# Kernel tuning notes

Hardware: AMD Instinct MI355X
Metric: run time of the kernel (lower is better)

The kernel has to match this reference:

```python
import jax, jax.numpy as jnp
import numpy as np

D = 48; N_IN = 8192; K = 24; RADIUS = 0.033
C_HID = 86; C_IN = 5; EMB = 16; MODES = 6; PAD = 6; N_LAYERS = 4
EPS = 1e-5


def _pos_embed(x):
    # neuraloperator PositionalEmbedding: scalar -> EMB channels (cos || sin)
    half = EMB // 2
    freqs = (1.0 / 10000.0) ** (jnp.arange(half, dtype=x.dtype) / half)
    ang = x[:, None] * freqs[None, :]
    return jnp.concatenate([jnp.cos(ang), jnp.sin(ang)], axis=-1)


def _gelu(x):
    return jax.nn.gelu(x, approximate=False)


def _conv1x1(h, w, b):
    return jnp.einsum('oi,ixyz->oxyz', w, h) + b[:, None, None, None]


def _group_norm(h, w, b):
    # GroupNorm(num_groups=1) on a batch-1 [C,X,Y,Z] tensor
    mu = jnp.mean(h)
    var = jnp.var(h)
    hn = (h - mu) * jax.lax.rsqrt(var + EPS)
    return hn * w[:, None, None, None] + b[:, None, None, None]


def _spectral_conv(h, wr, wi):
    S = h.shape[1]
    Xf = jnp.fft.rfftn(h, axes=(1, 2, 3))  # [C,S,S,S//2+1] complex64
    W = wr + 1j * wi                        # [4,C,C,m,m,m]
    out = jnp.zeros_like(Xf)
    m = MODES
    sls = (slice(0, m), slice(-m, None))
    c = 0
    for a in range(2):
        for b in range(2):
            blk = Xf[:, sls[a], sls[b], :m]
            res = jnp.einsum('ixyz,ioxyz->oxyz', blk, W[c])
            out = out.at[:, sls[a], sls[b], :m].set(res)
            c += 1
    return jnp.fft.irfftn(out, s=(S, S, S), axes=(1, 2, 3))


def _forward(x_in, x_out, df, w_lift, b_lift, spec_wr, spec_wi,
             w_skip, b_skip, mlp1_w, mlp1_b, mlp2_w, mlp2_b, wms, bms,
             g1_w, g1_b, g2_w, g2_b, k1_w, k1_b, k2_w, k2_b, k3_w, k3_b,
             p1_w, p1_b, p2_w, p2_b, nb_idx, nb_mask):
    n_out = D ** 3
    x_out_embed = _pos_embed(x_out.reshape(-1)).reshape(n_out, 3 * EMB)
    feat = jnp.concatenate([df, jnp.transpose(x_out, (3, 0, 1, 2))], axis=0)  # [5,D,D,D]
    h = _conv1x1(feat, w_lift, b_lift)
    h = jnp.pad(h, ((0, 0), (0, PAD), (0, PAD), (0, PAD)))  # one-sided domain padding
    for l in range(N_LAYERS):
        skip = _conv1x1(h, w_skip[l], b_skip[l])
        hf = _group_norm(_spectral_conv(h, spec_wr[l], spec_wi[l]), g1_w[l], g1_b[l])
        h = hf + skip
        if l < N_LAYERS - 1:
            h = _gelu(h)
        mskip = _conv1x1(h, wms[l], bms[l])
        hm = _conv1x1(_gelu(_conv1x1(h, mlp1_w[l], mlp1_b[l])), mlp2_w[l], mlp2_b[l])
        hm = _group_norm(hm, g2_w[l], g2_b[l])
        h = hm + mskip
        if l < N_LAYERS - 1:
            h = _gelu(h)
    h = h[:, :D, :D, :D]
    f_y = h.reshape(C_HID, n_out).T  # [n_out, C_HID]
    x_in_embed = _pos_embed(x_in.reshape(-1)).reshape(N_IN, 3 * EMB)
    # GNO: gather -> kernel MLP -> elementwise (linear kernel) -> mean scatter-reduce
    y_g = x_out_embed[nb_idx]                                        # [N,K,48]
    q_g = jnp.broadcast_to(x_in_embed[:, None, :], (N_IN, K, 3 * EMB))
    kin = jnp.concatenate([y_g, q_g], axis=-1)                       # [N,K,96]
    k = _gelu(kin @ k1_w.T + k1_b)
    k = _gelu(k @ k2_w.T + k2_b)
    k = k @ k3_w.T + k3_b                                            # [N,K,C_HID]
    f_g = f_y[nb_idx]                                                # [N,K,C_HID]
    mask = nb_mask[..., None].astype(k.dtype)
    num = jnp.sum(k * f_g * mask, axis=1)
    den = jnp.maximum(jnp.sum(nb_mask, axis=1), 1).astype(k.dtype)[:, None]
    out = num / den
    out = _gelu(out @ p1_w.T + p1_b)
    return out @ p2_w.T + p2_b                                       # [N,1]


def setup_inputs():
    rng = np.random.default_rng(0)
    lin = np.linspace(0.0, 1.0, D, dtype=np.float32)
    gx, gy, gz = np.meshgrid(lin, lin, lin, indexing='ij')
    x_out = np.stack([gx, gy, gz], axis=-1)                          # [D,D,D,3]
    x_in = rng.random((N_IN, 3)).astype(np.float32)
    # --- host-side ball-query neighbor search (regular grid, radius=RADIUS) ---
    spacing = 1.0 / (D - 1)
    rc = int(np.ceil(RADIUS / spacing))
    offs = np.arange(-rc, rc + 1)
    oi, oj, ok = np.meshgrid(offs, offs, offs, indexing='ij')
    offsets = np.stack([oi.ravel(), oj.ravel(), ok.ravel()], axis=-1)
    base = np.floor(x_in / spacing + 0.5).astype(np.int64)
    cand = base[:, None, :] + offsets[None, :, :]
    ok_v = np.all((cand >= 0) & (cand < D), axis=-1)
    cand = np.clip(cand, 0, D - 1)
    d2 = np.sum((cand.astype(np.float32) * spacing - x_in[:, None, :]) ** 2, axis=-1)
    inball = ok_v & (d2 <= RADIUS ** 2)
    order = np.argsort(~inball, axis=1, kind='stable')[:, :K]
    flat = (cand[..., 0] * D + cand[..., 1]) * D + cand[..., 2]
    nb_idx = np.take_along_axis(flat, order, axis=1).astype(np.int32)
    nb_mask = np.take_along_axis(inball, order, axis=1)

    def lw(o, i):
        return jnp.asarray((rng.standard_normal((o, i)) / np.sqrt(i)).astype(np.float32))

    def slw(n, o, i):
        return jnp.asarray((rng.standard_normal((n, o, i)) / np.sqrt(i)).astype(np.float32))

    m = MODES
    ss = 1.0 / C_HID
    spec_wr = jnp.asarray((rng.standard_normal((N_LAYERS, 4, C_HID, C_HID, m, m, m)) * ss).astype(np.float32))
    spec_wi = jnp.asarray((rng.standard_normal((N_LAYERS, 4, C_HID, C_HID, m, m, m)) * ss).astype(np.float32))
    zC = jnp.zeros((N_LAYERS, C_HID), dtype=jnp.float32)
    oC = jnp.ones((N_LAYERS, C_HID), dtype=jnp.float32)
    return dict(
        x_in=jnp.asarray(x_in), x_out=jnp.asarray(x_out),
        df=jnp.asarray(rng.standard_normal((C_IN - 3, D, D, D)).astype(np.float32)),
        nb_idx=jnp.asarray(nb_idx), nb_mask=jnp.asarray(nb_mask),
        w_lift=lw(C_HID, C_IN), b_lift=jnp.zeros(C_HID, dtype=jnp.float32),
        spec_wr=spec_wr, spec_wi=spec_wi,
        w_skip=slw(N_LAYERS, C_HID, C_HID), b_skip=zC,
        mlp1_w=slw(N_LAYERS, C_HID, C_HID), mlp1_b=zC,
        mlp2_w=slw(N_LAYERS, C_HID, C_HID), mlp2_b=zC,
        wms=slw(N_LAYERS, C_HID, C_HID), bms=zC,
        g1_w=oC, g1_b=zC, g2_w=oC, g2_b=zC,
        k1_w=lw(512, 6 * EMB), k1_b=jnp.zeros(512, dtype=jnp.float32),
        k2_w=lw(256, 512), k2_b=jnp.zeros(256, dtype=jnp.float32),
        k3_w=lw(C_HID, 256), k3_b=jnp.zeros(C_HID, dtype=jnp.float32),
        p1_w=lw(256, C_HID), p1_b=jnp.zeros(256, dtype=jnp.float32),
        p2_w=lw(1, 256), p2_b=jnp.zeros(1, dtype=jnp.float32),
    )


def reference(x_in, x_out, df, nb_idx, nb_mask, w_lift, b_lift, spec_wr, spec_wi,
              w_skip, b_skip, mlp1_w, mlp1_b, mlp2_w, mlp2_b, wms, bms,
              g1_w, g1_b, g2_w, g2_b, k1_w, k1_b, k2_w, k2_b, k3_w, k3_b,
              p1_w, p1_b, p2_w, p2_b):
    return _forward(x_in, x_out, df, w_lift, b_lift, spec_wr, spec_wi,
                    w_skip, b_skip, mlp1_w, mlp1_b, mlp2_w, mlp2_b, wms, bms,
                    g1_w, g1_b, g2_w, g2_b, k1_w, k1_b, k2_w, k2_b, k3_w, k3_b,
                    p1_w, p1_b, p2_w, p2_b, nb_idx, nb_mask)
```

## Files before the change

### kernel.cpp

```cpp
#include <hip/hip_runtime.h>
#include <math.h>

#define CH 86
#define SP 54
#define SS2 2916
#define SS3 157464
#define DG 48
#define MPAD 157568
#define RT_ROWS (CH*SS2)
#define NSLICE (CH*SP)
#define PI_F 3.14159265358979323846f
#define GN_INV (1.0/13541904.0)

static constexpr size_t A512(size_t x){ return (x + 511) & ~((size_t)511); }
static constexpr size_t HBYTES = (size_t)CH*SS3*4;
static constexpr size_t ABYTES = (size_t)MPAD*96*2;
static constexpr size_t XBYTES = (size_t)MPAD*96*4;
static constexpr size_t FAB = (size_t)CH*SS2*6*8;
static constexpr size_t FBB = (size_t)CH*SP*12*6*8;
static constexpr size_t FCB = (size_t)CH*864*8;
static constexpr size_t OFF_HA = 0;
static constexpr size_t OFF_HS = OFF_HA + A512(HBYTES);
static constexpr size_t OFF_AB = OFF_HS + A512(HBYTES);
static constexpr size_t OFF_BB = OFF_AB + A512(ABYTES);
static constexpr size_t OFF_TB = OFF_BB + A512(ABYTES);
static constexpr size_t OFF_XSC= OFF_TB + A512(ABYTES);
static constexpr size_t OFF_FA = OFF_XSC+ A512(XBYTES);
static constexpr size_t OFF_FB = OFF_FA + A512(FAB);
static constexpr size_t OFF_FC = OFF_FB + A512(FBB);
static constexpr size_t OFF_FD = OFF_FC + A512(FCB);
static constexpr size_t OFF_FE = OFF_FD + A512(FCB);
static constexpr size_t OFF_ST = OFF_FE + A512(FBB);
static constexpr size_t OFF_WB = OFF_ST + 512;
static constexpr size_t OFF_K3 = OFF_WB + A512((size_t)16*96*96*2);
static constexpr int    CHUNK_M = 98304;
static constexpr size_t OFF_KIN = 0;
static constexpr size_t OFF_Z1  = A512((size_t)CHUNK_M*96*2);
static constexpr size_t OFF_Z2  = OFF_Z1 + A512((size_t)CHUNK_M*512*2);
static constexpr size_t OFF_W1  = OFF_Z2 + A512((size_t)CHUNK_M*256*2);
static constexpr size_t OFF_W2  = OFF_W1 + A512((size_t)512*96*2);
static constexpr size_t OFF_W3  = OFF_W2 + A512((size_t)256*512*2);

typedef __attribute__((ext_vector_type(8))) short bf16x8;
typedef __attribute__((ext_vector_type(4))) float f32x4;

__device__ __forceinline__ float gelu_f(float x){
  return 0.5f*x*(1.0f + erff(x*0.70710678118654752440f));
}
__device__ __forceinline__ unsigned short f2bf(float x){
  unsigned u = __float_as_uint(x);
  u += 0x7fffu + ((u>>16)&1u);
  return (unsigned short)(u>>16);
}

__global__ void k_zero_stats(double* st){ if (threadIdx.x < 16) st[threadIdx.x] = 0.0; }

__global__ __launch_bounds__(256) void k_f2bf(const float* __restrict__ in,
    unsigned short* __restrict__ out, int n)
{
  int i = blockIdx.x*256 + threadIdx.x;
  if (i < n) out[i] = f2bf(in[i]);
}

__global__ __launch_bounds__(256) void k_wprep(const float* __restrict__ src,
    unsigned short* __restrict__ dst, int slot)
{
  int l = blockIdx.y;
  int idx = blockIdx.x*256 + threadIdx.x;
  int n = idx/96, k = idx-96*n;
  unsigned short v = 0;
  if (n < 86 && k < 86) v = f2bf(src[(size_t)l*7396 + n*86 + k]);
  dst[(size_t)(l*4+slot)*9216 + idx] = v;
}

__global__ __launch_bounds__(256) void k_lift(const float* __restrict__ df,
    const float* __restrict__ wl, const float* __restrict__ bl,
    float* __restrict__ hA, unsigned short* __restrict__ Ab)
{
  __shared__ float vals[128*96];
  const int t = threadIdx.x;
  const int s0 = blockIdx.x*128;
  for(int idx=t; idx<128*96; idx+=256){
    int sl = idx/96, o = idx-96*sl;
    int s = s0+sl;
    float v = 0.f;
    if (o < 86){
      int x = s/2916, r2 = s-2916*x, y = r2/54, z = r2-54*y;
      if (x<DG && y<DG && z<DG){
        int p = (x*DG + y)*DG + z;
        v = wl[o*5]*df[p] + wl[o*5+1]*df[110592+p]
          + wl[o*5+2]*(x*(1.0f/47.0f)) + wl[o*5+3]*(y*(1.0f/47.0f))
          + wl[o*5+4]*(z*(1.0f/47.0f)) + bl[o];
      }
    }
    vals[idx] = v;
  }
  __syncthreads();
  for(int idx=t; idx<128*96; idx+=256)
    Ab[(size_t)s0*96 + idx] = f2bf(vals[idx]);
  for(int idx=t; idx<86*128; idx+=256){
    int c = idx/128, sl = idx-128*c;
    int s = s0+sl;
    if (s < SS3) hA[(size_t)c*SS3 + s] = vals[sl*96 + c];
  }
}

__global__ __launch_bounds__(256) void k_dft_z(const float* __restrict__ h, float* __restrict__ A)
{
  __shared__ alignas(16) float rows[64*55];
  __shared__ float twc[6*54], tws[6*54];
  const int t = threadIdx.x;
  for(int idx=t; idx<6*54; idx+=256){
    int k = idx/54, z = idx-54*k;
    int m = (k*z)%54;
    float ang = -(2.0f*PI_F/54.0f)*(float)m;
    twc[idx]=cosf(ang); tws[idx]=sinf(ang);
  }
  const int r0 = blockIdx.x*64;
  for(int idx=t; idx<64*54; idx+=256){
    int r = idx/54;
    rows[r*55 + (idx-54*r)] = (r0+r < RT_ROWS)? h[(size_t)r0*54 + idx] : 0.f;
  }
  __syncthreads();
  for(int oi=t; oi<768; oi+=256){
    int r = oi & 63;
    int k = (oi>>6)%6;
    int part = oi/384;
    if (r0+r < RT_ROWS){
      const float* tw = part? tws : twc;
      const float* rp = &rows[r*55];
      const float* twk = &tw[k*54];
      float acc=0.f;
      #pragma unroll 6
      for(int z=0;z<54;z++) acc += rp[z]*twk[z];
      A[((size_t)(r0+r)*6 + k)*2 + part] = acc;
    }
  }
}

__global__ __launch_bounds__(256) void k_dft_y(const float* __restrict__ A, float* __restrict__ B)
{
  __shared__ float asl[4*648];
  __shared__ float twc[12*54], tws[12*54];
  const int t = threadIdx.x;
  for(int idx=t; idx<12*54; idx+=256){
    int kyi = idx/54, y = idx-54*kyi;
    int ky = (kyi<6)? kyi : (42+kyi);
    int m = (ky*y)%54;
    float ang = -(2.0f*PI_F/54.0f)*(float)m;
    twc[idx]=cosf(ang); tws[idx]=sinf(ang);
  }
  const int s0 = blockIdx.x*4;
  for(int idx=t; idx<4*648; idx+=256){
    int sl = idx/648;
    asl[idx] = (s0+sl < NSLICE)? A[(size_t)s0*648 + idx] : 0.f;
  }
  __syncthreads();
  for(int oi=t; oi<4*72; oi+=256){
    int sl = oi/72, o = oi-72*sl;
    if (s0+sl >= NSLICE) continue;
    int kyi = o/6, kz = o-6*kyi;
    const float* base = &asl[sl*648];
    float cr=0.f, ci=0.f;
    for(int y=0;y<54;y++){
      float ar = base[(y*6+kz)*2], ai = base[(y*6+kz)*2+1];
      float tc = twc[kyi*54+y], ts = tws[kyi*54+y];
      cr += ar*tc - ai*ts;
      ci += ar*ts + ai*tc;
    }
    size_t ob = ((size_t)(s0+sl)*12 + kyi)*6 + kz;
    B[ob*2]=cr; B[ob*2+1]=ci;
  }
}

__global__ __launch_bounds__(256) void k_dft_x(const float* __restrict__ B, float* __restrict__ C)
{
  __shared__ float bsl[7776];
  __shared__ float twc[12*54], tws[12*54];
  const int t = threadIdx.x;
  const int i = blockIdx.x;
  for(int idx=t; idx<12*54; idx+=256){
    int kxi = idx/54, x = idx-54*kxi;
    int kx = (kxi<6)? kxi : (42+kxi);
    int m = (kx*x)%54;
    float ang = -(2.0f*PI_F/54.0f)*(float)m;
    twc[idx]=cosf(ang); tws[idx]=sinf(ang);
  }
  for(int idx=t; idx<7776; idx+=256) bsl[idx] = B[(size_t)i*7776 + idx];
  __syncthreads();
  for(int oi=t; oi<864; oi+=256){
    int kxi = oi/72, rest = oi-72*kxi;
    float cr=0.f, ci=0.f;
    for(int x=0;x<54;x++){
      float br = bsl[(x*72+rest)*2], bi = bsl[(x*72+rest)*2+1];
      float tc = twc[kxi*54+x], ts = tws[kxi*54+x];
      cr += br*tc - bi*ts;
      ci += br*ts + bi*tc;
    }
    int kyi = rest/6, kz = rest-6*kyi;
    int c = ((kxi>=6)?2:0) + ((kyi>=6)?1:0);
    int f = ((kxi%6)*6 + (kyi%6))*6 + kz;
    size_t ob = ((size_t)i*4 + c)*216 + f;
    C[ob*2]=cr; C[ob*2+1]=ci;
  }
// ... 60 lines not shown
{
  __shared__ float esl[4*144];
  __shared__ float twc[12*54], tws[12*54];
  const int t = threadIdx.x;
  for(int idx=t; idx<12*54; idx+=256){
    int kyi = idx/54, y = idx-54*kyi;
    int ky = (kyi<6)? kyi : (42+kyi);
    int m = (ky*y)%54;
    float ang = (2.0f*PI_F/54.0f)*(float)m;
    twc[idx]=cosf(ang); tws[idx]=sinf(ang);
  }
  const int s0 = blockIdx.x*4;
  for(int idx=t; idx<4*144; idx+=256){
    int sl = idx/144;
    esl[idx] = (s0+sl < NSLICE)? E[(size_t)s0*144 + idx] : 0.f;
  }
  __syncthreads();
  for(int oi=t; oi<4*324; oi+=256){
    int sl = oi/324, rest = oi-324*sl;
    if (s0+sl >= NSLICE) continue;
    int y = rest/6, kz = rest-6*y;
    const float* base = &esl[sl*144];
    float fr=0.f, fi=0.f;
    #pragma unroll
    for(int kyi=0;kyi<12;kyi++){
      float er = base[(kyi*6+kz)*2], ei = base[(kyi*6+kz)*2+1];
      float tc = twc[kyi*54+y], ts = tws[kyi*54+y];
      fr += er*tc - ei*ts;
      fi += er*ts + ei*tc;
    }
    size_t ob = ((size_t)(s0+sl)*54 + y)*6 + kz;
    F[ob*2]=fr; F[ob*2+1]=fi;
  }
}

__global__ __launch_bounds__(256) void k_idft_z(const float* __restrict__ F,
    float* __restrict__ hs, double* __restrict__ st)
{
  __shared__ float rws[64*12];
  __shared__ float twc[5*54], tws[5*54];
  __shared__ float red[8];
  const int t = threadIdx.x;
  for(int idx=t; idx<5*54; idx+=256){
    int k = idx/54 + 1, z = idx%54;
    int m = (k*z)%54;
    float ang = (2.0f*PI_F/54.0f)*(float)m;
    twc[idx]=cosf(ang); tws[idx]=sinf(ang);
  }
  const int r0 = blockIdx.x*64;
  for(int idx=t; idx<768; idx+=256){
    int r = idx/12;
    rws[idx] = (r0+r < RT_ROWS)? F[(size_t)r0*12 + idx] : 0.f;
  }
  __syncthreads();
  const float inv = 1.0f/157464.0f;
  float lsum=0.f, lsq=0.f;
  for(int oi=t; oi<64*54; oi+=256){
    int r = oi/54, z = oi-54*r;
    if (r0+r < RT_ROWS){
      const float* fr = &rws[r*12];
      float acc = fr[0];
      #pragma unroll
      for(int k=1;k<=5;k++)
        acc += 2.0f*(fr[2*k]*twc[(k-1)*54+z] - fr[2*k+1]*tws[(k-1)*54+z]);
      acc *= inv;
      hs[(size_t)r0*54 + oi] = acc;
      lsum += acc; lsq += acc*acc;
    }
  }
  #pragma unroll
  for(int off=32; off; off>>=1){
    lsum += __shfl_down(lsum, off, 64);
    lsq  += __shfl_down(lsq,  off, 64);
  }
  if ((t&63)==0){ red[(t>>6)*2]=lsum; red[(t>>6)*2+1]=lsq; }
  __syncthreads();
  if (t==0){
    double s1 = (double)red[0]+red[2]+red[4]+red[6];
    double s2 = (double)red[1]+red[3]+red[5]+red[7];
    atomicAdd(st, s1); atomicAdd(st+1, s2);
  }
}

template<int ACT, int ADDN, int OSTAT, int OB, int OCS, int OSC>
__global__ __launch_bounds__(256) void k_convm(
    const unsigned short* __restrict__ Ain, const unsigned short* __restrict__ Wb,
    const float* __restrict__ bias,
    const float* __restrict__ Xcs, const float* __restrict__ Xsc,
    const float* __restrict__ g, const float* __restrict__ bg,
    const double* __restrict__ ist, double* __restrict__ ost,
    unsigned short* __restrict__ outb, float* __restrict__ outcs, float* __restrict__ outsc)
{
  __shared__ unsigned short As[128*32];
  __shared__ unsigned short Bs[96*32];
  __shared__ float red[8];
  const int t = threadIdx.x, lane = t&63, w = t>>6;
  const int m0 = blockIdx.x*128;
  const int lr = lane>>2, lq = lane&3;
  f32x4 acc[2][6];
  #pragma unroll
  for(int s=0;s<2;s++)
    #pragma unroll
    for(int n=0;n<6;n++) acc[s][n] = (f32x4){0.f,0.f,0.f,0.f};

  #pragma unroll
  for(int k0=0;k0<96;k0+=32){
    __syncthreads();
    #pragma unroll
    for(int j=0;j<4;j++){
      int slot = j*4 + w;
      if (slot < 8){
        int row = slot*16 + lr;
        const unsigned short* ga = Ain + (size_t)(m0+row)*96 + k0 + lq*8;
        __builtin_amdgcn_global_load_lds((const __attribute__((address_space(1))) void*)ga,
            (__attribute__((address_space(3))) void*)&As[slot*512], 16, 0, 0);
      } else if (slot < 14){
        int bs = slot-8;
        int row = bs*16 + lr;
        const unsigned short* gb = Wb + (size_t)row*96 + k0 + lq*8;
        __builtin_amdgcn_global_load_lds((const __attribute__((address_space(1))) void*)gb,
            (__attribute__((address_space(3))) void*)&Bs[bs*512], 16, 0, 0);
      }
    }
    __syncthreads();
    bf16x8 af[2], bf[6];
    #pragma unroll
    for(int s=0;s<2;s++)
      af[s] = *(const bf16x8*)&As[(w*32 + s*16 + (lane&15))*32 + (lane>>4)*8];
    #pragma unroll
    for(int n=0;n<6;n++)
      bf[n] = *(const bf16x8*)&Bs[(n*16 + (lane&15))*32 + (lane>>4)*8];
    #pragma unroll
    for(int s=0;s<2;s++)
      #pragma unroll
      for(int n=0;n<6;n++)
        acc[s][n] = __builtin_amdgcn_mfma_f32_16x16x32_bf16(af[s], bf[n], acc[s][n], 0, 0, 0);
  }

  float mu=0.f, rs=1.f;
  if (ADDN){
    double m = ist[0]*GN_INV;
    double v = ist[1]*GN_INV - m*m;
    mu = (float)m;
    rs = (float)(1.0/sqrt(v + 1e-5));
  }
  float lsum=0.f, lsq=0.f;
  const int colb = lane&15, rowq = (lane>>4)*4;
  #pragma unroll
  for(int n=0;n<6;n++){
    int col = n*16 + colb;
    bool cv = (col < CH);
    float bn=0.f, gg=1.f, bb=0.f;
    if (cv){
      bn = bias[col];
      if (ADDN){ gg = g[col]; bb = bg[col]; }
    }
    #pragma unroll
    for(int s=0;s<2;s++){
      #pragma unroll
      for(int r=0;r<4;r++){
        int row = m0 + w*32 + s*16 + rowq + r;
        float v = 0.f;
        if (cv){
          v = acc[s][n][r] + bn;
          if (ADDN==1){ if (row < SS3) v += (Xcs[(size_t)col*SS3 + row]-mu)*rs*gg + bb; }
          if (ADDN==2){ v += (Xsc[(size_t)row*96 + col]-mu)*rs*gg + bb; }
          if (ACT) v = gelu_f(v);
          if (OSTAT){ if (row < SS3){ lsum += v; lsq += v*v; } }
        }
        if (OB) outb[(size_t)row*96 + col] = f2bf(v);
        if (OCS){ if (cv && row < SS3) outcs[(size_t)col*SS3 + row] = v; }
        if (OSC) outsc[(size_t)row*96 + col] = v;
      }
    }
  }
  if (OSTAT){
    #pragma unroll
    for(int off=32; off; off>>=1){
      lsum += __shfl_down(lsum, off, 64);
      lsq  += __shfl_down(lsq,  off, 64);
    }
    if ((lane)==0){ red[w*2]=lsum; red[w*2+1]=lsq; }
    __syncthreads();
    if (t==0){
      double s1 = (double)red[0]+red[2]+red[4]+red[6];
      double s2 = (double)red[1]+red[3]+red[5]+red[7];
      atomicAdd(ost, s1); atomicAdd(ost+1, s2);
    }
  }
}

__global__ __launch_bounds__(256) void k_build_kin(const float* __restrict__ x_in,
    const int* __restrict__ nb_idx, unsigned short* __restrict__ kin, int pair0)
{
  int gidx = blockIdx.x*256 + threadIdx.x;
  int lp = gidx/96, col = gidx - lp*96;
  int pair = pair0 + lp;
  int qi = pair/24;
  int cc = col; bool isq = false;
  if (cc >= 48){ cc -= 48; isq = true; }
  int ci = cc>>4, e = cc&15;
  int f = e&7; bool is_sin = (e>=8);
  float coord;
  if (isq){
    coord = x_in[qi*3 + ci];
  } else {
    int pt = nb_idx[pair];
    int gcoord;
    if (ci==0) gcoord = pt/2304;
    else if (ci==1) gcoord = (pt/48)%48;
    else gcoord = pt%48;
    coord = gcoord*(1.0f/47.0f);
  }
  float freq = exp2f(-(float)f * 1.66096404744368117f);
  float ang = coord*freq;
  kin[gidx] = f2bf(is_sin ? sinf(ang) : cosf(ang));
}

template<int ACT, int OUT_BF16>
__global__ __launch_bounds__(256,2) void k_gemm_mfma(
    const unsigned short* __restrict__ A, const unsigned short* __restrict__ B,
    const float* __restrict__ bias, void* __restrict__ Cout,
    int M, int N, int K)
{
  __shared__ unsigned short As[128*32];
  __shared__ unsigned short Bs[128*32];
  const int t = threadIdx.x;
  const int lane = t & 63, w = t >> 6;
  const int wm = w >> 1, wn = w & 1;
  const int m0 = blockIdx.x*128, n0 = blockIdx.y*128;
  const int lr = lane >> 2, lq = lane & 3;
  f32x4 acc[4][4];
  #pragma unroll
  for(int s=0;s<4;s++)
    #pragma unroll
    for(int n=0;n<4;n++) acc[s][n] = (f32x4){0.f,0.f,0.f,0.f};

  for(int k0=0;k0<K;k0+=32){
    __syncthreads();
    #pragma unroll
    for(int j=0;j<2;j++){
      int slot = w*2 + j;
      int row = slot*16 + lr;
      const unsigned short* ga = A + (size_t)(m0+row)*K + k0 + lq*8;
      __builtin_amdgcn_global_load_lds((const __attribute__((address_space(1))) void*)ga,
          (__attribute__((address_space(3))) void*)&As[slot*512], 16, 0, 0);
      int brow = n0 + row; if (brow > N-1) brow = N-1;
      const unsigned short* gb = B + (size_t)brow*K + k0 + lq*8;
      __builtin_amdgcn_global_load_lds((const __attribute__((address_space(1))) void*)gb,
          (__attribute__((address_space(3))) void*)&Bs[slot*512], 16, 0, 0);
    }
    __syncthreads();
    bf16x8 af[4], bg[4];
    #pragma unroll
    for(int s=0;s<4;s++)
      af[s] = *(const bf16x8*)&As[(wm*64 + s*16 + (lane&15))*32 + (lane>>4)*8];
    #pragma unroll
    for(int n=0;n<4;n++)
      bg[n] = *(const bf16x8*)&Bs[(wn*64 + n*16 + (lane&15))*32 + (lane>>4)*8];
    #pragma unroll
    for(int s=0;s<4;s++)
      #pragma unroll
      for(int n=0;n<4;n++)
        acc[s][n] = __builtin_amdgcn_mfma_f32_16x16x32_bf16(af[s], bg[n], acc[s][n], 0, 0, 0);
  }

  unsigned short* Cb = (unsigned short*)Cout;
  float* Cf = (float*)Cout;
  const int colb = n0 + wn*64 + (lane&15);
  const int rowb = m0 + wm*64 + (lane>>4)*4;
  #pragma unroll
  for(int n=0;n<4;n++){
    int col = colb + n*16;
    if (col < N){
      float bn = bias[col];
      #pragma unroll
      for(int s=0;s<4;s++){
        int row = rowb + s*16;
        #pragma unroll
        for(int r=0;r<4;r++){
          float v = acc[s][n][r] + bn;
          if (ACT) v = gelu_f(v);
          if (OUT_BF16) Cb[(size_t)(row+r)*N + col] = f2bf(v);
          else          Cf[(size_t)(row+r)*N + col] = v;
        }
      }
    }
  }
}

__global__ __launch_bounds__(256) void k_gno_reduce(
    const float* __restrict__ K3, const float* __restrict__ FY,
    const int* __restrict__ nb_idx, const int* __restrict__ nb_mask,
    const float* __restrict__ p1w, const float* __restrict__ p1b,
    const float* __restrict__ p2w, const float* __restrict__ p2b,
    float* __restrict__ out)
{
  __shared__ float v[CH];
  __shared__ int   sidx[24];
  __shared__ float smk[24];
  __shared__ float red[4];
  const int i = blockIdx.x, t = threadIdx.x;
  if (t < 24){
    int pt = nb_idx[i*24+t];
    int x = pt/2304, rem = pt-2304*x, y = rem/48, z = rem-48*y;
    sidx[t] = x*2916 + y*54 + z;
    smk[t]  = (nb_mask[i*24+t] != 0)? 1.f : 0.f;
  }
  __syncthreads();
  if (t < CH){
    float acc=0.f, den=0.f;
    for(int k=0;k<24;k++){
      float m = smk[k];
      den += m;
      if (m > 0.f)
        acc += K3[((size_t)(i*24+k))*CH + t]*FY[(size_t)sidx[k]*96 + t];
    }
    if (den < 1.f) den = 1.f;
    v[t] = acc/den;
  }
  __syncthreads();
  float a1 = p1b[t];
  for(int c=0;c<CH;c++) a1 += v[c]*p1w[t*CH + c];
  float part = gelu_f(a1)*p2w[t];
  #pragma unroll
  for(int off=32; off; off>>=1) part += __shfl_down(part, off, 64);
  if ((t&63)==0) red[t>>6] = part;
  __syncthreads();
  if (t==0) out[i] = red[0]+red[1]+red[2]+red[3] + p2b[0];
}

extern "C" void kernel_launch(void* const* d_in, const int* in_sizes, int n_in,
                              void* d_out, int out_size, void* d_ws, size_t ws_size,
                              hipStream_t stream)
{
  (void)in_sizes; (void)n_in; (void)out_size; (void)ws_size;
  const float* x_in  = (const float*)d_in[0];
  const float* df    = (const float*)d_in[2];
  const int*   nbidx = (const int*)d_in[3];
  const int*   nbmsk = (const int*)d_in[4];
  const float* wlift = (const float*)d_in[5];
  const float* blift = (const float*)d_in[6];
  const float* spwr  = (const float*)d_in[7];
  const float* spwi  = (const float*)d_in[8];
  const float* wskip = (const float*)d_in[9];
  const float* bskip = (const float*)d_in[10];
  const float* m1w   = (const float*)d_in[11];
  const float* m1b   = (const float*)d_in[12];
  const float* m2w   = (const float*)d_in[13];
  const float* m2b   = (const float*)d_in[14];
  const float* wms   = (const float*)d_in[15];
  const float* bms   = (const float*)d_in[16];
  const float* g1w   = (const float*)d_in[17];
  const float* g1b   = (const float*)d_in[18];
  const float* g2w   = (const float*)d_in[19];
  const float* g2b   = (const float*)d_in[20];
  const float* k1w   = (const float*)d_in[21];
  const float* k1b   = (const float*)d_in[22];
  const float* k2w   = (const float*)d_in[23];
  const float* k2b   = (const float*)d_in[24];
  const float* k3w   = (const float*)d_in[25];
  const float* k3b   = (const float*)d_in[26];
  const float* p1w   = (const float*)d_in[27];
  const float* p1b   = (const float*)d_in[28];
  const float* p2w   = (const float*)d_in[29];
  const float* p2b   = (const float*)d_in[30];
  float* out = (float*)d_out;
  char* ws = (char*)d_ws;

  float* hA = (float*)(ws + OFF_HA);
  float* hS = (float*)(ws + OFF_HS);
  unsigned short* Ab = (unsigned short*)(ws + OFF_AB);
  unsigned short* Bb = (unsigned short*)(ws + OFF_BB);
  unsigned short* Tb = (unsigned short*)(ws + OFF_TB);
  float* Xsc = (float*)(ws + OFF_XSC);
  float* fA = (float*)(ws + OFF_FA);
  float* fB = (float*)(ws + OFF_FB);
  float* fC = (float*)(ws + OFF_FC);
  float* fD = (float*)(ws + OFF_FD);
  float* fE = (float*)(ws + OFF_FE);
  double* st= (double*)(ws + OFF_ST);
  unsigned short* Wb = (unsigned short*)(ws + OFF_WB);
  float* K3 = (float*)(ws + OFF_K3);
  unsigned short* kinb = (unsigned short*)(ws + OFF_KIN);
  unsigned short* Z1b  = (unsigned short*)(ws + OFF_Z1);
  unsigned short* Z2b  = (unsigned short*)(ws + OFF_Z2);
  unsigned short* w1b  = (unsigned short*)(ws + OFF_W1);
  unsigned short* w2b  = (unsigned short*)(ws + OFF_W2);
  unsigned short* w3b  = (unsigned short*)(ws + OFF_W3);

  k_zero_stats<<<1,64,0,stream>>>(st);
  k_wprep<<<dim3(36,4),256,0,stream>>>(wskip, Wb, 0);
  k_wprep<<<dim3(36,4),256,0,stream>>>(m1w,   Wb, 1);
  k_wprep<<<dim3(36,4),256,0,stream>>>(m2w,   Wb, 2);
  k_wprep<<<dim3(36,4),256,0,stream>>>(wms,   Wb, 3);
  k_lift<<<1231,256,0,stream>>>(df, wlift, blift, hA, Ab);

  for(int l=0;l<4;l++){
    const float* wr_l = spwr + (size_t)l*4*CH*CH*216;
    const float* wi_l = spwi + (size_t)l*4*CH*CH*216;
    double* st1 = st + l*4;
    double* st2 = st + l*4 + 2;
    k_dft_z<<<3919,256,0,stream>>>(hA, fA);
    k_dft_y<<<1161,256,0,stream>>>(fA, fB);
    k_dft_x<<<86,256,0,stream>>>(fB, fC);
    k_mix<<<dim3(86,4),256,0,stream>>>(fC, wr_l, wi_l, fD);
    k_idft_x<<<86,256,0,stream>>>(fD, fE);
    k_idft_y<<<1161,256,0,stream>>>(fE, fA);
    k_idft_z<<<3919,256,0,stream>>>(fA, hS, st1);
    const unsigned short* Wskip = Wb + (size_t)(l*4+0)*9216;
    const unsigned short* Wm1   = Wb + (size_t)(l*4+1)*9216;
    const unsigned short* Wm2   = Wb + (size_t)(l*4+2)*9216;
    const unsigned short* Wms   = Wb + (size_t)(l*4+3)*9216;
    if (l<3) k_convm<1,1,0,1,0,0><<<1231,256,0,stream>>>(Ab, Wskip, bskip+l*86, hS, nullptr, g1w+l*86, g1b+l*86, st1, nullptr, Bb, nullptr, nullptr);
    else     k_convm<0,1,0,1,0,0><<<1231,256,0,stream>>>(Ab, Wskip, bskip+l*86, hS, nullptr, g1w+l*86, g1b+l*86, st1, nullptr, Bb, nullptr, nullptr);
    k_convm<1,0,0,1,0,0><<<1231,256,0,stream>>>(Bb, Wm1, m1b+l*86, nullptr, nullptr, nullptr, nullptr, nullptr, nullptr, Tb, nullptr, nullptr);
    k_convm<0,0,1,0,0,1><<<1231,256,0,stream>>>(Tb, Wm2, m2b+l*86, nullptr, nullptr, nullptr, nullptr, nullptr, st2, nullptr, nullptr, Xsc);
    if (l<3) k_convm<1,2,0,1,1,0><<<1231,256,0,stream>>>(Bb, Wms, bms+l*86, nullptr, Xsc, g2w+l*86, g2b+l*86, st2, nullptr, Ab, hA, nullptr);
    else     k_convm<0,2,0,0,0,1><<<1231,256,0,stream>>>(Bb, Wms, bms+l*86, nullptr, Xsc, g2w+l*86, g2b+l*86, st2, nullptr, nullptr, nullptr, Xsc);
  }

  k_f2bf<<<(512*96+255)/256,256,0,stream>>>(k1w, w1b, 512*96);
  k_f2bf<<<(256*512+255)/256,256,0,stream>>>(k2w, w2b, 256*512);
  k_f2bf<<<(86*256+255)/256,256,0,stream>>>(k3w, w3b, 86*256);

  for(int ch=0; ch<2; ch++){
    int pair0 = ch*CHUNK_M;
    k_build_kin<<<(CHUNK_M*96)/256,256,0,stream>>>(x_in, nbidx, kinb, pair0);
    k_gemm_mfma<1,1><<<dim3(CHUNK_M/128,4),256,0,stream>>>(kinb, w1b, k1b, (void*)Z1b, CHUNK_M, 512, 96);
    k_gemm_mfma<1,1><<<dim3(CHUNK_M/128,2),256,0,stream>>>(Z1b, w2b, k2b, (void*)Z2b, CHUNK_M, 256, 512);
    k_gemm_mfma<0,0><<<dim3(CHUNK_M/128,1),256,0,stream>>>(Z2b, w3b, k3b, (void*)(K3 + (size_t)pair0*CH), CHUNK_M, 86, 256);
  }

  k_gno_reduce<<<8192,256,0,stream>>>(K3, Xsc, nbidx, nbmsk, p1w, p1b, p2w, p2b, out);
}
```

Measured before the change: 2.411 ms.

## Fuse skip/MLP conv chain into one kernel, store spectral input as bf16, MFMA projection

```diff
diff --git a/kernel.cpp b/kernel.cpp
--- a/kernel.cpp
+++ b/kernel.cpp
@@ -13,33 +13,36 @@
 #define GN_INV (1.0/13541904.0)
 
 static constexpr size_t A512(size_t x){ return (x + 511) & ~((size_t)511); }
-static constexpr size_t HBYTES = (size_t)CH*SS3*4;
-static constexpr size_t ABYTES = (size_t)MPAD*96*2;
-static constexpr size_t XBYTES = (size_t)MPAD*96*4;
+static constexpr size_t HB2 = (size_t)CH*SS3*2;
+static constexpr size_t HB4 = (size_t)CH*SS3*4;
+static constexpr size_t AB2 = (size_t)MPAD*96*2;
+static constexpr size_t XB4 = (size_t)MPAD*96*4;
 static constexpr size_t FAB = (size_t)CH*SS2*6*8;
 static constexpr size_t FBB = (size_t)CH*SP*12*6*8;
 static constexpr size_t FCB = (size_t)CH*864*8;
 static constexpr size_t OFF_HA = 0;
-static constexpr size_t OFF_HS = OFF_HA + A512(HBYTES);
-static constexpr size_t OFF_AB = OFF_HS + A512(HBYTES);
-static constexpr size_t OFF_BB = OFF_AB + A512(ABYTES);
-static constexpr size_t OFF_TB = OFF_BB + A512(ABYTES);
-static constexpr size_t OFF_XSC= OFF_TB + A512(ABYTES);
-static constexpr size_t OFF_FA = OFF_XSC+ A512(XBYTES);
+static constexpr size_t OFF_HS = OFF_HA + A512(HB2);
+static constexpr size_t OFF_AB = OFF_HS + A512(HB4);
+static constexpr size_t OFF_BB = OFF_AB + A512(AB2);
+static constexpr size_t OFF_XSC= OFF_BB + A512(AB2);
+static constexpr size_t OFF_FA = OFF_XSC+ A512(XB4);
 static constexpr size_t OFF_FB = OFF_FA + A512(FAB);
 static constexpr size_t OFF_FC = OFF_FB + A512(FBB);
 static constexpr size_t OFF_FD = OFF_FC + A512(FCB);
 static constexpr size_t OFF_FE = OFF_FD + A512(FCB);
 static constexpr size_t OFF_ST = OFF_FE + A512(FBB);
 static constexpr size_t OFF_WB = OFF_ST + 512;
-static constexpr size_t OFF_K3 = OFF_WB + A512((size_t)16*96*96*2);
+static constexpr size_t OFF_P1W= OFF_WB + A512((size_t)16*96*96*2);
+static constexpr size_t OFF_W1 = OFF_P1W+ A512((size_t)256*96*2);
+static constexpr size_t OFF_W2 = OFF_W1 + A512((size_t)512*96*2);
+static constexpr size_t OFF_W3 = OFF_W2 + A512((size_t)256*512*2);
+static constexpr size_t OFF_K3 = OFF_W3 + A512((size_t)86*256*2);
+static constexpr size_t OFF_Z2 = OFF_K3 + A512((size_t)196608*CH*4);
+static constexpr size_t OFF_U  = OFF_Z2 + A512((size_t)98304*256*2);
+static constexpr size_t OFF_H1 = OFF_U  + A512((size_t)8192*96*2);
 static constexpr int    CHUNK_M = 98304;
 static constexpr size_t OFF_KIN = 0;
 static constexpr size_t OFF_Z1  = A512((size_t)CHUNK_M*96*2);
-static constexpr size_t OFF_Z2  = OFF_Z1 + A512((size_t)CHUNK_M*512*2);
-static constexpr size_t OFF_W1  = OFF_Z2 + A512((size_t)CHUNK_M*256*2);
-static constexpr size_t OFF_W2  = OFF_W1 + A512((size_t)512*96*2);
-static constexpr size_t OFF_W3  = OFF_W2 + A512((size_t)256*512*2);
 
 typedef __attribute__((ext_vector_type(8))) short bf16x8;
 typedef __attribute__((ext_vector_type(4))) float f32x4;
@@ -51,6 +54,9 @@
   unsigned u = __float_as_uint(x);
   u += 0x7fffu + ((u>>16)&1u);
   return (unsigned short)(u>>16);
+}
+__device__ __forceinline__ float bf2f(unsigned short u){
+  return __uint_as_float(((unsigned)u)<<16);
 }
 
 __global__ void k_zero_stats(double* st){ if (threadIdx.x < 16) st[threadIdx.x] = 0.0; }
@@ -73,9 +79,18 @@
   dst[(size_t)(l*4+slot)*9216 + idx] = v;
 }
 
+__global__ __launch_bounds__(256) void k_pad_w(const float* __restrict__ src,
+    unsigned short* __restrict__ dst, int rows)
+{
+  int idx = blockIdx.x*256 + threadIdx.x;
+  if (idx >= rows*96) return;
+  int n = idx/96, k = idx-96*n;
+  dst[idx] = (k<86)? f2bf(src[n*86+k]) : (unsigned short)0;
+}
+
 __global__ __launch_bounds__(256) void k_lift(const float* __restrict__ df,
     const float* __restrict__ wl, const float* __restrict__ bl,
-    float* __restrict__ hA, unsigned short* __restrict__ Ab)
+    unsigned short* __restrict__ hA, unsigned short* __restrict__ Ab)
 {
   __shared__ float vals[128*96];
   const int t = threadIdx.x;
@@ -101,11 +116,11 @@
   for(int idx=t; idx<86*128; idx+=256){
     int c = idx/128, sl = idx-128*c;
     int s = s0+sl;
-    if (s < SS3) hA[(size_t)c*SS3 + s] = vals[sl*96 + c];
-  }
-}
-
-__global__ __launch_bounds__(256) void k_dft_z(const float* __restrict__ h, float* __restrict__ A)
+    if (s < SS3) hA[(size_t)c*SS3 + s] = f2bf(vals[sl*96 + c]);
+  }
+}
+
+__global__ __launch_bounds__(256) void k_dft_z(const unsigned short* __restrict__ h, float* __restrict__ A)
 {
   __shared__ alignas(16) float rows[64*55];
   __shared__ float twc[6*54], tws[6*54];
@@ -119,7 +134,7 @@
   const int r0 = blockIdx.x*64;
   for(int idx=t; idx<64*54; idx+=256){
     int r = idx/54;
-    rows[r*55 + (idx-54*r)] = (r0+r < RT_ROWS)? h[(size_t)r0*54 + idx] : 0.f;
+    rows[r*55 + (idx-54*r)] = (r0+r < RT_ROWS)? bf2f(h[(size_t)r0*54 + idx]) : 0.f;
   }
   __syncthreads();
   for(int oi=t; oi<768; oi+=256){
@@ -346,79 +361,164 @@
   }
 }
 
-template<int ACT, int ADDN, int OSTAT, int OB, int OCS, int OSC>
-__global__ __launch_bounds__(256) void k_convm(
-    const unsigned short* __restrict__ Ain, const unsigned short* __restrict__ Wb,
-    const float* __restrict__ bias,
-    const float* __restrict__ Xcs, const float* __restrict__ Xsc,
-    const float* __restrict__ g, const float* __restrict__ bg,
-    const double* __restrict__ ist, double* __restrict__ ost,
-    unsigned short* __restrict__ outb, float* __restrict__ outcs, float* __restrict__ outsc)
-{
-  __shared__ unsigned short As[128*32];
-  __shared__ unsigned short Bs[96*32];
+template<int ACT1>
+__global__ __launch_bounds__(256) void k_fuse3(
+    const unsigned short* __restrict__ Ain, const unsigned short* __restrict__ Wl3,
+    const float* __restrict__ bsk, const float* __restrict__ b1,
+    const float* __restrict__ b2,
+    const float* __restrict__ hS, const float* __restrict__ g1,
+    const float* __restrict__ bg1, const double* __restrict__ st1,
+    double* __restrict__ st2,
+    unsigned short* __restrict__ Bb, float* __restrict__ Hm)
+{
+  __shared__ unsigned short Wl[96*96];
+  __shared__ unsigned short Achunk[8*512];
+  __shared__ unsigned short Tt[128*96];
   __shared__ float red[8];
   const int t = threadIdx.x, lane = t&63, w = t>>6;
   const int m0 = blockIdx.x*128;
   const int lr = lane>>2, lq = lane&3;
+  const int colb = lane&15, rowq = (lane>>4)*4;
   f32x4 acc[2][6];
+
+  for(int s=w; s<18; s+=4){
+    const unsigned short* gw = Wl3 + s*512 + lane*8;
+    __builtin_amdgcn_global_load_lds((const __attribute__((address_space(1))) void*)gw,
+        (__attribute__((address_space(3))) void*)&Wl[s*512], 16, 0, 0);
+  }
   #pragma unroll
   for(int s=0;s<2;s++)
     #pragma unroll
     for(int n=0;n<6;n++) acc[s][n] = (f32x4){0.f,0.f,0.f,0.f};
-
   #pragma unroll
   for(int k0=0;k0<96;k0+=32){
     __syncthreads();
     #pragma unroll
-    for(int j=0;j<4;j++){
-      int slot = j*4 + w;
-      if (slot < 8){
-        int row = slot*16 + lr;
-        const unsigned short* ga = Ain + (size_t)(m0+row)*96 + k0 + lq*8;
-        __builtin_amdgcn_global_load_lds((const __attribute__((address_space(1))) void*)ga,
-            (__attribute__((address_space(3))) void*)&As[slot*512], 16, 0, 0);
-      } else if (slot < 14){
-        int bs = slot-8;
-        int row = bs*16 + lr;
-        const unsigned short* gb = Wb + (size_t)row*96 + k0 + lq*8;
-        __builtin_amdgcn_global_load_lds((const __attribute__((address_space(1))) void*)gb,
-            (__attribute__((address_space(3))) void*)&Bs[bs*512], 16, 0, 0);
-      }
+    for(int j=0;j<2;j++){
+      int slot = w*2+j;
+      int row = slot*16 + lr;
+      const unsigned short* ga = Ain + (size_t)(m0+row)*96 + k0 + lq*8;
+      __builtin_amdgcn_global_load_lds((const __attribute__((address_space(1))) void*)ga,
+          (__attribute__((address_space(3))) void*)&Achunk[slot*512], 16, 0, 0);
     }
     __syncthreads();
     bf16x8 af[2], bf[6];
     #pragma unroll
     for(int s=0;s<2;s++)
-      af[s] = *(const bf16x8*)&As[(w*32 + s*16 + (lane&15))*32 + (lane>>4)*8];
+      af[s] = *(const bf16x8*)&Achunk[(w*32 + s*16 + (lane&15))*32 + (lane>>4)*8];
     #pragma unroll
     for(int n=0;n<6;n++)
-      bf[n] = *(const bf16x8*)&Bs[(n*16 + (lane&15))*32 + (lane>>4)*8];
+      bf[n] = *(const bf16x8*)&Wl[(n*16 + (lane&15))*96 + k0 + (lane>>4)*8];
     #pragma unroll
     for(int s=0;s<2;s++)
       #pragma unroll
       for(int n=0;n<6;n++)
         acc[s][n] = __builtin_amdgcn_mfma_f32_16x16x32_bf16(af[s], bf[n], acc[s][n], 0, 0, 0);
   }
-
-  float mu=0.f, rs=1.f;
-  if (ADDN){
-    double m = ist[0]*GN_INV;
-    double v = ist[1]*GN_INV - m*m;
-    mu = (float)m;
-    rs = (float)(1.0/sqrt(v + 1e-5));
-  }
-  float lsum=0.f, lsq=0.f;
-  const int colb = lane&15, rowq = (lane>>4)*4;
+  {
+    double m = st1[0]*GN_INV;
+    double va = st1[1]*GN_INV - m*m;
+    float mu = (float)m, rs = (float)(1.0/sqrt(va + 1e-5));
+    #pragma unroll
+    for(int n=0;n<6;n++){
+      int col = n*16 + colb;
+      bool cv = (col < CH);
+      float bn=0.f, gg=1.f, bb=0.f;
+      if (cv){ bn = bsk[col]; gg = g1[col]; bb = bg1[col]; }
+      #pragma unroll
+      for(int s=0;s<2;s++){
+        #pragma unroll
+        for(int r=0;r<4;r++){
+          int rowl = w*32 + s*16 + rowq + r;
+          int row = m0 + rowl;
+          float v = 0.f;
+          if (cv){
+            v = acc[s][n][r] + bn;
+            if (row < SS3) v += (hS[(size_t)col*SS3 + row]-mu)*rs*gg + bb;
+            if (ACT1) v = gelu_f(v);
+          }
+          unsigned short vb = f2bf(v);
+          Bb[(size_t)row*96 + col] = vb;
+          Tt[rowl*96 + col] = vb;
+        }
+      }
+    }
+  }
+
+  __syncthreads();
+  for(int s=w; s<18; s+=4){
+    const unsigned short* gw = Wl3 + 9216 + s*512 + lane*8;
+    __builtin_amdgcn_global_load_lds((const __attribute__((address_space(1))) void*)gw,
+        (__attribute__((address_space(3))) void*)&Wl[s*512], 16, 0, 0);
+  }
+  #pragma unroll
+  for(int s=0;s<2;s++)
+    #pragma unroll
+    for(int n=0;n<6;n++) acc[s][n] = (f32x4){0.f,0.f,0.f,0.f};
+  __syncthreads();
+  #pragma unroll
+  for(int k0=0;k0<96;k0+=32){
+    bf16x8 af[2], bf[6];
+    #pragma unroll
+    for(int s=0;s<2;s++)
+      af[s] = *(const bf16x8*)&Tt[(w*32 + s*16 + (lane&15))*96 + k0 + (lane>>4)*8];
+    #pragma unroll
+    for(int n=0;n<6;n++)
+      bf[n] = *(const bf16x8*)&Wl[(n*16 + (lane&15))*96 + k0 + (lane>>4)*8];
+    #pragma unroll
+    for(int s=0;s<2;s++)
+      #pragma unroll
+      for(int n=0;n<6;n++)
+        acc[s][n] = __builtin_amdgcn_mfma_f32_16x16x32_bf16(af[s], bf[n], acc[s][n], 0, 0, 0);
+  }
   #pragma unroll
   for(int n=0;n<6;n++){
     int col = n*16 + colb;
     bool cv = (col < CH);
-    float bn=0.f, gg=1.f, bb=0.f;
-    if (cv){
-      bn = bias[col];
-      if (ADDN){ gg = g[col]; bb = bg[col]; }
-    }
+    float bn = cv? b1[col] : 0.f;
+    #pragma unroll
+    for(int s=0;s<2;s++){
+      #pragma unroll
+      for(int r=0;r<4;r++){
+        int rowl = w*32 + s*16 + rowq + r;
+        float v = cv? gelu_f(acc[s][n][r] + bn) : 0.f;
+        Tt[rowl*96 + col] = f2bf(v);
+      }
+    }
+  }
+
+  __syncthreads();
+  for(int s=w; s<18; s+=4){
+    const unsigned short* gw = Wl3 + 18432 + s*512 + lane*8;
+    __builtin_amdgcn_global_load_lds((const __attribute__((address_space(1))) void*)gw,
+        (__attribute__((address_space(3))) void*)&Wl[s*512], 16, 0, 0);
+  }
+  #pragma unroll
+  for(int s=0;s<2;s++)
+    #pragma unroll
+    for(int n=0;n<6;n++) acc[s][n] = (f32x4){0.f,0.f,0.f,0.f};
+  __syncthreads();
+  #pragma unroll
+  for(int k0=0;k0<96;k0+=32){
+    bf16x8 af[2], bf[6];
+    #pragma unroll
+    for(int s=0;s<2;s++)
+      af[s] = *(const bf16x8*)&Tt[(w*32 + s*16 + (lane&15))*96 + k0 + (lane>>4)*8];
+    #pragma unroll
+    for(int n=0;n<6;n++)
+      bf[n] = *(const bf16x8*)&Wl[(n*16 + (lane&15))*96 + k0 + (lane>>4)*8];
+    #pragma unroll
+    for(int s=0;s<2;s++)
+      #pragma unroll
+      for(int n=0;n<6;n++)
+        acc[s][n] = __builtin_amdgcn_mfma_f32_16x16x32_bf16(af[s], bf[n], acc[s][n], 0, 0, 0);
+  }
+  float lsum=0.f, lsq=0.f;
+  #pragma unroll
+  for(int n=0;n<6;n++){
+    int col = n*16 + colb;
+    bool cv = (col < CH);
+    float bn = cv? b2[col] : 0.f;
     #pragma unroll
     for(int s=0;s<2;s++){
       #pragma unroll
@@ -427,29 +527,102 @@
         float v = 0.f;
         if (cv){
           v = acc[s][n][r] + bn;
-          if (ADDN==1){ if (row < SS3) v += (Xcs[(size_t)col*SS3 + row]-mu)*rs*gg + bb; }
-          if (ADDN==2){ v += (Xsc[(size_t)row*96 + col]-mu)*rs*gg + bb; }
-          if (ACT) v = gelu_f(v);
-          if (OSTAT){ if (row < SS3){ lsum += v; lsq += v*v; } }
+          if (row < SS3){ lsum += v; lsq += v*v; }
         }
-        if (OB) outb[(size_t)row*96 + col] = f2bf(v);
-        if (OCS){ if (cv && row < SS3) outcs[(size_t)col*SS3 + row] = v; }
-        if (OSC) outsc[(size_t)row*96 + col] = v;
+        Hm[(size_t)row*96 + col] = v;
       }
     }
   }
-  if (OSTAT){
-    #pragma unroll
-    for(int off=32; off; off>>=1){
-      lsum += __shfl_down(lsum, off, 64);
-      lsq  += __shfl_down(lsq,  off, 64);
-    }
-    if ((lane)==0){ red[w*2]=lsum; red[w*2+1]=lsq; }
+  #pragma unroll
+  for(int off=32; off; off>>=1){
+    lsum += __shfl_down(lsum, off, 64);
+    lsq  += __shfl_down(lsq,  off, 64);
+  }
+  if (lane==0){ red[w*2]=lsum; red[w*2+1]=lsq; }
+  __syncthreads();
+  if (t==0){
+    double s1 = (double)red[0]+red[2]+red[4]+red[6];
+    double s2 = (double)red[1]+red[3]+red[5]+red[7];
+    atomicAdd(st2, s1); atomicAdd(st2+1, s2);
+  }
+}
+
+template<int LAST>
+__global__ __launch_bounds__(256) void k_convms(
+    const unsigned short* __restrict__ Ain, const unsigned short* __restrict__ Wm,
+    const float* __restrict__ bms,
+    const float* __restrict__ Hm, const float* __restrict__ g2,
+    const float* __restrict__ bg2, const double* __restrict__ st2,
+    unsigned short* __restrict__ Ab, unsigned short* __restrict__ hA,
+    float* __restrict__ FY)
+{
+  __shared__ unsigned short Wl[96*96];
+  __shared__ unsigned short Achunk[8*512];
+  const int t = threadIdx.x, lane = t&63, w = t>>6;
+  const int m0 = blockIdx.x*128;
+  const int lr = lane>>2, lq = lane&3;
+  for(int s=w; s<18; s+=4){
+    const unsigned short* gw = Wm + s*512 + lane*8;
+    __builtin_amdgcn_global_load_lds((const __attribute__((address_space(1))) void*)gw,
+        (__attribute__((address_space(3))) void*)&Wl[s*512], 16, 0, 0);
+  }
+  f32x4 acc[2][6];
+  #pragma unroll
+  for(int s=0;s<2;s++)
+    #pragma unroll
+    for(int n=0;n<6;n++) acc[s][n] = (f32x4){0.f,0.f,0.f,0.f};
+  #pragma unroll
+  for(int k0=0;k0<96;k0+=32){
     __syncthreads();
-    if (t==0){
-      double s1 = (double)red[0]+red[2]+red[4]+red[6];
-      double s2 = (double)red[1]+red[3]+red[5]+red[7];
-      atomicAdd(ost, s1); atomicAdd(ost+1, s2);
+    #pragma unroll
+    for(int j=0;j<2;j++){
+      int slot = w*2+j;
+      int row = slot*16 + lr;
+      const unsigned short* ga = Ain + (size_t)(m0+row)*96 + k0 + lq*8;
+      __builtin_amdgcn_global_load_lds((const __attribute__((address_space(1))) void*)ga,
+          (__attribute__((address_space(3))) void*)&Achunk[slot*512], 16, 0, 0);
+    }
+    __syncthreads();
+    bf16x8 af[2], bf[6];
+    #pragma unroll
+    for(int s=0;s<2;s++)
+      af[s] = *(const bf16x8*)&Achunk[(w*32 + s*16 + (lane&15))*32 + (lane>>4)*8];
+    #pragma unroll
+    for(int n=0;n<6;n++)
+      bf[n] = *(const bf16x8*)&Wl[(n*16 + (lane&15))*96 + k0 + (lane>>4)*8];
+    #pragma unroll
+    for(int s=0;s<2;s++)
+      #pragma unroll
+      for(int n=0;n<6;n++)
+        acc[s][n] = __builtin_amdgcn_mfma_f32_16x16x32_bf16(af[s], bf[n], acc[s][n], 0, 0, 0);
+  }
+  double m = st2[0]*GN_INV;
+  double va = st2[1]*GN_INV - m*m;
+  float mu = (float)m, rs = (float)(1.0/sqrt(va + 1e-5));
+  const int colb = lane&15, rowq = (lane>>4)*4;
+  #pragma unroll
+  for(int n=0;n<6;n++){
+    int col = n*16 + colb;
+    bool cv = (col < CH);
+    float bn=0.f, gg=1.f, bb=0.f;
+    if (cv){ bn = bms[col]; gg = g2[col]; bb = bg2[col]; }
+    #pragma unroll
+    for(int s=0;s<2;s++){
+      #pragma unroll
+      for(int r=0;r<4;r++){
+        int row = m0 + w*32 + s*16 + rowq + r;
+        float v = 0.f;
+        if (cv){
+          v = acc[s][n][r] + bn + (Hm[(size_t)row*96 + col]-mu)*rs*gg + bb;
+          if (!LAST) v = gelu_f(v);
+        }
+        if (LAST){
+          FY[(size_t)row*96 + col] = v;
+        } else {
+          Ab[(size_t)row*96 + col] = f2bf(v);
+          if (cv && row < SS3) hA[(size_t)col*SS3 + row] = f2bf(v);
+        }
+      }
     }
   }
 }
@@ -553,45 +726,54 @@
   }
 }
 
-__global__ __launch_bounds__(256) void k_gno_reduce(
+__global__ __launch_bounds__(256) void k_gno_u(
     const float* __restrict__ K3, const float* __restrict__ FY,
     const int* __restrict__ nb_idx, const int* __restrict__ nb_mask,
-    const float* __restrict__ p1w, const float* __restrict__ p1b,
+    unsigned short* __restrict__ U)
+{
+  __shared__ int sidx[4][24];
+  __shared__ float smk[4][24];
+  const int t = threadIdx.x, w = t>>6, lane = t&63;
+  const int i0 = blockIdx.x*4;
+  if (t < 96){
+    int q = t/24, k = t-24*q;
+    int pt = nb_idx[(i0+q)*24+k];
+    int x = pt/2304, rem = pt-2304*x, y = rem/48, z = rem-48*y;
+    sidx[q][k] = x*2916 + y*54 + z;
+    smk[q][k] = (nb_mask[(i0+q)*24+k] != 0)? 1.f : 0.f;
+  }
+  __syncthreads();
+  const int i = i0 + w;
+  const int c1 = lane, c2 = 64+lane;
+  float a1=0.f, a2=0.f, den=0.f;
+  for(int k=0;k<24;k++){
+    float mk = smk[w][k];
+    den += mk;
+    if (mk > 0.f){
+      const float* k3p = K3 + (size_t)(i*24+k)*CH;
+      const float* fyp = FY + (size_t)sidx[w][k]*96;
+      a1 += k3p[c1]*fyp[c1];
+      if (c2 < CH) a2 += k3p[c2]*fyp[c2];
+    }
+  }
+  if (den < 1.f) den = 1.f;
+  U[(size_t)i*96 + c1] = f2bf(a1/den);
+  if (c2 < 96) U[(size_t)i*96 + c2] = f2bf((c2 < CH)? a2/den : 0.f);
+}
+
+__global__ __launch_bounds__(256) void k_out(const unsigned short* __restrict__ H1,
     const float* __restrict__ p2w, const float* __restrict__ p2b,
     float* __restrict__ out)
 {
-  __shared__ float v[CH];
-  __shared__ int   sidx[24];
-  __shared__ float smk[24];
-  __shared__ float red[4];
-  const int i = blockIdx.x, t = threadIdx.x;
-  if (t < 24){
-    int pt = nb_idx[i*24+t];
-    int x = pt/2304, rem = pt-2304*x, y = rem/48, z = rem-48*y;
-    sidx[t] = x*2916 + y*54 + z;
-    smk[t]  = (nb_mask[i*24+t] != 0)? 1.f : 0.f;
-  }
-  __syncthreads();
-  if (t < CH){
-    float acc=0.f, den=0.f;
-    for(int k=0;k<24;k++){
-      float m = smk[k];
-      den += m;
-      if (m > 0.f)
-        acc += K3[((size_t)(i*24+k))*CH + t]*FY[(size_t)sidx[k]*96 + t];
-    }
-    if (den < 1.f) den = 1.f;
-    v[t] = acc/den;
-  }
-  __syncthreads();
-  float a1 = p1b[t];
-  for(int c=0;c<CH;c++) a1 += v[c]*p1w[t*CH + c];
-  float part = gelu_f(a1)*p2w[t];
-  #pragma unroll
-  for(int off=32; off; off>>=1) part += __shfl_down(part, off, 64);
-  if ((t&63)==0) red[t>>6] = part;
-  __syncthreads();
-  if (t==0) out[i] = red[0]+red[1]+red[2]+red[3] + p2b[0];
+  const int t = threadIdx.x, w = t>>6, lane = t&63;
+  const int i = blockIdx.x*4 + w;
+  const unsigned short* hp = H1 + (size_t)i*256 + lane*4;
+  float s = 0.f;
+  #pragma unroll
+  for(int j=0;j<4;j++) s += bf2f(hp[j]) * p2w[lane*4+j];
+  #pragma unroll
+  for(int off=32; off; off>>=1) s += __shfl_down(s, off, 64);
+  if (lane==0) out[i] = s + p2b[0];
 }
 
 extern "C" void kernel_launch(void* const* d_in, const int* in_sizes, int n_in,
@@ -632,11 +814,10 @@
   float* out = (float*)d_out;
   char* ws = (char*)d_ws;
 
-  float* hA = (float*)(ws + OFF_HA);
+  unsigned short* hAb = (unsigned short*)(ws + OFF_HA);
   float* hS = (float*)(ws + OFF_HS);
   unsigned short* Ab = (unsigned short*)(ws + OFF_AB);
   unsigned short* Bb = (unsigned short*)(ws + OFF_BB);
-  unsigned short* Tb = (unsigned short*)(ws + OFF_TB);
   float* Xsc = (float*)(ws + OFF_XSC);
   float* fA = (float*)(ws + OFF_FA);
   float* fB = (float*)(ws + OFF_FB);
@@ -645,48 +826,54 @@
   float* fE = (float*)(ws + OFF_FE);
   double* st= (double*)(ws + OFF_ST);
   unsigned short* Wb = (unsigned short*)(ws + OFF_WB);
-  float* K3 = (float*)(ws + OFF_K3);
-  unsigned short* kinb = (unsigned short*)(ws + OFF_KIN);
-  unsigned short* Z1b  = (unsigned short*)(ws + OFF_Z1);
-  unsigned short* Z2b  = (unsigned short*)(ws + OFF_Z2);
+  unsigned short* p1wb = (unsigned short*)(ws + OFF_P1W);
   unsigned short* w1b  = (unsigned short*)(ws + OFF_W1);
   unsigned short* w2b  = (unsigned short*)(ws + OFF_W2);
   unsigned short* w3b  = (unsigned short*)(ws + OFF_W3);
+  float* K3 = (float*)(ws + OFF_K3);
+  unsigned short* Z2b  = (unsigned short*)(ws + OFF_Z2);
+  unsigned short* Ub   = (unsigned short*)(ws + OFF_U);
+  unsigned short* H1b  = (unsigned short*)(ws + OFF_H1);
+  unsigned short* kinb = (unsigned short*)(ws + OFF_KIN);
+  unsigned short* Z1b  = (unsigned short*)(ws + OFF_Z1);
 
   k_zero_stats<<<1,64,0,stream>>>(st);
   k_wprep<<<dim3(36,4),256,0,stream>>>(wskip, Wb, 0);
   k_wprep<<<dim3(36,4),256,0,stream>>>(m1w,   Wb, 1);
   k_wprep<<<dim3(36,4),256,0,stream>>>(m2w,   Wb, 2);
   k_wprep<<<dim3(36,4),256,0,stream>>>(wms,   Wb, 3);
-  k_lift<<<1231,256,0,stream>>>(df, wlift, blift, hA, Ab);
+  k_pad_w<<<96,256,0,stream>>>(p1w, p1wb, 256);
+  k_f2bf<<<(512*96+255)/256,256,0,stream>>>(k1w, w1b, 512*96);
+  k_f2bf<<<(256*512+255)/256,256,0,stream>>>(k2w, w2b, 256*512);
+  k_f2bf<<<(86*256+255)/256,256,0,stream>>>(k3w, w3b, 86*256);
+  k_lift<<<1231,256,0,stream>>>(df, wlift, blift, hAb, Ab);
 
   for(int l=0;l<4;l++){
     const float* wr_l = spwr + (size_t)l*4*CH*CH*216;
     const float* wi_l = spwi + (size_t)l*4*CH*CH*216;
     double* st1 = st + l*4;
     double* st2 = st + l*4 + 2;
-    k_dft_z<<<3919,256,0,stream>>>(hA, fA);
+    k_dft_z<<<3919,256,0,stream>>>(hAb, fA);
     k_dft_y<<<1161,256,0,stream>>>(fA, fB);
     k_dft_x<<<86,256,0,stream>>>(fB, fC);
     k_mix<<<dim3(86,4),256,0,stream>>>(fC, wr_l, wi_l, fD);
     k_idft_x<<<86,256,0,stream>>>(fD, fE);
     k_idft_y<<<1161,256,0,stream>>>(fE, fA);
     k_idft_z<<<3919,256,0,stream>>>(fA, hS, st1);
-    const unsigned short* Wskip = Wb + (size_t)(l*4+0)*9216;
-    const unsigned short* Wm1   = Wb + (size_t)(l*4+1)*9216;
-    const unsigned short* Wm2   = Wb + (size_t)(l*4+2)*9216;
-    const unsigned short* Wms   = Wb + (size_t)(l*4+3)*9216;
-    if (l<3) k_convm<1,1,0,1,0,0><<<1231,256,0,stream>>>(Ab, Wskip, bskip+l*86, hS, nullptr, g1w+l*86, g1b+l*86, st1, nullptr, Bb, nullptr, nullptr);
-    else     k_convm<0,1,0,1,0,0><<<1231,256,0,stream>>>(Ab, Wskip, bskip+l*86, hS, nullptr, g1w+l*86, g1b+l*86, st1, nullptr, Bb, nullptr, nullptr);
-    k_convm<1,0,0,1,0,0><<<1231,256,0,stream>>>(Bb, Wm1, m1b+l*86, nullptr, nullptr, nullptr, nullptr, nullptr, nullptr, Tb, nullptr, nullptr);
-    k_convm<0,0,1,0,0,1><<<1231,256,0,stream>>>(Tb, Wm2, m2b+l*86, nullptr, nullptr, nullptr, nullptr, nullptr, st2, nullptr, nullptr, Xsc);
-    if (l<3) k_convm<1,2,0,1,1,0><<<1231,256,0,stream>>>(Bb, Wms, bms+l*86, nullptr, Xsc, g2w+l*86, g2b+l*86, st2, nullptr, Ab, hA, nullptr);
-    else     k_convm<0,2,0,0,0,1><<<1231,256,0,stream>>>(Bb, Wms, bms+l*86, nullptr, Xsc, g2w+l*86, g2b+l*86, st2, nullptr, nullptr, nullptr, Xsc);
-  }
-
-  k_f2bf<<<(512*96+255)/256,256,0,stream>>>(k1w, w1b, 512*96);
-  k_f2bf<<<(256*512+255)/256,256,0,stream>>>(k2w, w2b, 256*512);
-  k_f2bf<<<(86*256+255)/256,256,0,stream>>>(k3w, w3b, 86*256);
+    const unsigned short* Wl3 = Wb + (size_t)l*4*9216;
+    const unsigned short* Wms = Wb + (size_t)(l*4+3)*9216;
+    if (l<3){
+      k_fuse3<1><<<1231,256,0,stream>>>(Ab, Wl3, bskip+l*86, m1b+l*86, m2b+l*86,
+          hS, g1w+l*86, g1b+l*86, st1, st2, Bb, Xsc);
+      k_convms<0><<<1231,256,0,stream>>>(Bb, Wms, bms+l*86, Xsc, g2w+l*86, g2b+l*86,
+          st2, Ab, hAb, nullptr);
+    } else {
+      k_fuse3<0><<<1231,256,0,stream>>>(Ab, Wl3, bskip+l*86, m1b+l*86, m2b+l*86,
+          hS, g1w+l*86, g1b+l*86, st1, st2, Bb, Xsc);
+      k_convms<1><<<1231,256,0,stream>>>(Bb, Wms, bms+l*86, Xsc, g2w+l*86, g2b+l*86,
+          st2, nullptr, nullptr, Xsc);
+    }
+  }
 
   for(int ch=0; ch<2; ch++){
     int pair0 = ch*CHUNK_M;
@@ -696,5 +883,7 @@
     k_gemm_mfma<0,0><<<dim3(CHUNK_M/128,1),256,0,stream>>>(Z2b, w3b, k3b, (void*)(K3 + (size_t)pair0*CH), CHUNK_M, 86, 256);
   }
 
-  k_gno_reduce<<<8192,256,0,stream>>>(K3, Xsc, nbidx, nbmsk, p1w, p1b, p2w, p2b, out);
-}
+  k_gno_u<<<2048,256,0,stream>>>(K3, Xsc, nbidx, nbmsk, Ub);
+  k_gemm_mfma<1,1><<<dim3(64,2),256,0,stream>>>(Ub, p1wb, p1b, (void*)H1b, 8192, 256, 96);
+  k_out<<<2048,256,0,stream>>>(H1b, p2w, p2b, out);
+}
```

New measurement: 2.205 ms. 8.5% less time.
